# Optimization experiments

Measured on AMD Instinct MI355X. Metric: run time of the kernel, lower is better.

Reference implementation:

```python
import jax, jax.numpy as jnp
import numpy as np

C = 512
GROUPS = 8
EPS = 1e-5


def setup_inputs() -> dict:
    key = jax.random.key(0)
    ks = jax.random.split(key, 7)
    b, c, h, w = 32, C, 32, 32
    x = jax.random.normal(ks[0], (b, c, h, w), dtype=jnp.float32)
    norm_gamma = jnp.ones((c,), dtype=jnp.float32)
    norm_beta = jnp.zeros((c,), dtype=jnp.float32)
    # 1x1 convs == per-pixel linear layers; store as [out, in] matrices
    qkv_w = jax.random.normal(ks[1], (3 * c, c), dtype=jnp.float32) * (1.0 / np.sqrt(c))
    qkv_b = jnp.zeros((3 * c,), dtype=jnp.float32)
    out_w = jax.random.normal(ks[2], (c, c), dtype=jnp.float32) * (1.0 / np.sqrt(c))
    out_b = jnp.zeros((c,), dtype=jnp.float32)
    return {"x": x, "norm_gamma": norm_gamma, "norm_beta": norm_beta,
            "qkv_w": qkv_w, "qkv_b": qkv_b, "out_w": out_w, "out_b": out_b}


def group_norm(x, gamma, beta):
    b, c, h, w = x.shape
    xg = x.reshape(b, GROUPS, c // GROUPS, h, w)
    mean = jnp.mean(xg, axis=(2, 3, 4), keepdims=True)
    var = jnp.var(xg, axis=(2, 3, 4), keepdims=True)
    xg = (xg - mean) * jax.lax.rsqrt(var + EPS)
    x = xg.reshape(b, c, h, w)
    return x * gamma[None, :, None, None] + beta[None, :, None, None]


def reference(x, norm_gamma, norm_beta, qkv_w, qkv_b, out_w, out_b):
    b, c, h, w = x.shape
    xn = group_norm(x, norm_gamma, norm_beta)
    # 1x1 conv: [b,c,h,w] -> [b,3c,h,w]
    qkv = jnp.einsum('oc,bchw->bohw', qkv_w, xn) + qkv_b[None, :, None, None]
    q, k, v = jnp.split(qkv.reshape(b, 3 * c, h * w), 3, axis=1)  # each [b,c,hw]
    scale = c ** (-0.5)
    attn = jnp.einsum('bci,bcj->bij', q, k) * scale  # [b, hw, hw]
    attn = jax.nn.softmax(attn, axis=-1)
    out = jnp.einsum('bij,bcj->bci', attn, v).reshape(b, c, h, w)
    out = jnp.einsum('oc,bchw->bohw', out_w, out) + out_b[None, :, None, None]
    return x + out
```

## Files before the change

### kernel.cpp

```cpp
#include <hip/hip_runtime.h>

#define HW 1024
#define CD 512

typedef __bf16 bf16x8 __attribute__((ext_vector_type(8)));
typedef float f32x4 __attribute__((ext_vector_type(4)));

__device__ __forceinline__ unsigned short f2bf(float f) {
    unsigned int u = __float_as_uint(f);
    u += 0x7fff + ((u >> 16) & 1);
    return (unsigned short)(u >> 16);
}
__device__ __forceinline__ float bf2f(unsigned short h) {
    return __uint_as_float((unsigned)h << 16);
}

#define AS1(p) ((__attribute__((address_space(1))) void*)(p))
#define AS3(p) ((__attribute__((address_space(3))) void*)(p))
#define GLD16(gp, lp) __builtin_amdgcn_global_load_lds(AS1(gp), AS3(lp), 16, 0, 0)
#define WAITVM(n) do { asm volatile("s_waitcnt vmcnt(" #n ")" ::: "memory"); \
                       __builtin_amdgcn_sched_barrier(0); } while (0)

__global__ __launch_bounds__(256)
void gn_stats(const float* __restrict__ x, float* __restrict__ mean, float* __restrict__ rstd) {
    int bg = blockIdx.x;
    const float4* p4 = (const float4*)(x + (size_t)bg * 65536);
    int tid = threadIdx.x;
    float s = 0.f, ss = 0.f;
#pragma unroll 8
    for (int it = 0; it < 64; ++it) {
        float4 v = p4[tid + it * 256];
        s  += v.x + v.y + v.z + v.w;
        ss += v.x * v.x + v.y * v.y + v.z * v.z + v.w * v.w;
    }
#pragma unroll
    for (int d = 32; d > 0; d >>= 1) { s += __shfl_down(s, d); ss += __shfl_down(ss, d); }
    __shared__ float ls[4], lss[4];
    if ((tid & 63) == 0) { ls[tid >> 6] = s; lss[tid >> 6] = ss; }
    __syncthreads();
    if (tid == 0) {
        float S = ls[0] + ls[1] + ls[2] + ls[3];
        float SS = lss[0] + lss[1] + lss[2] + lss[3];
        float m = S * (1.f / 65536.f);
        float v = SS * (1.f / 65536.f) - m * m;
        mean[bg] = m;
        rstd[bg] = rsqrtf(v + 1e-5f);
    }
}

__global__ __launch_bounds__(256)
void gn_norm_t(const float* __restrict__ x, const float* __restrict__ mean, const float* __restrict__ rstd,
               const float* __restrict__ gamma, const float* __restrict__ beta,
               unsigned short* __restrict__ xnT) {
    __shared__ unsigned short tile[64][67];
    int i0 = blockIdx.x * 64, c0 = blockIdx.y * 64, b = blockIdx.z;
    float m = mean[b * 8 + blockIdx.y];
    float r = rstd[b * 8 + blockIdx.y];
    int tid = threadIdx.x;
    int tr = tid >> 4, tc = (tid & 15) * 4;
    const float* xb = x + ((size_t)b * CD + c0) * HW + i0;
#pragma unroll
    for (int p = 0; p < 4; ++p) {
        int c = tr + p * 16;
        float g = gamma[c0 + c] * r;
        float bb = beta[c0 + c] - m * g;
        float4 v = *(const float4*)(xb + (size_t)c * HW + tc);
        tile[c][tc + 0] = f2bf(v.x * g + bb);
        tile[c][tc + 1] = f2bf(v.y * g + bb);
        tile[c][tc + 2] = f2bf(v.z * g + bb);
        tile[c][tc + 3] = f2bf(v.w * g + bb);
    }
    __syncthreads();
    unsigned short* ob = xnT + ((size_t)b * HW + i0) * CD + c0;
#pragma unroll
    for (int p = 0; p < 4; ++p) {
        int ir = tr + p * 16;
        ushort4 u;
        u.x = tile[tc + 0][ir];
        u.y = tile[tc + 1][ir];
        u.z = tile[tc + 2][ir];
        u.w = tile[tc + 3][ir];
        *(ushort4*)(ob + (size_t)ir * CD + tc) = u;
    }
}

__global__ __launch_bounds__(256)
void tpose3_bf16(const float* __restrict__ qkv_w, unsigned short* __restrict__ dst0) {
    __shared__ unsigned short tile[64][67];
    const int zmap[3] = {0, 2, 1};
    const float* src = qkv_w + (size_t)blockIdx.z * CD * CD;
    unsigned short* dst = dst0 + (size_t)zmap[blockIdx.z] * CD * CD;
    int i0 = blockIdx.x * 64, c0 = blockIdx.y * 64;
    int tid = threadIdx.x;
    int tr = tid >> 4, tc = (tid & 15) * 4;
#pragma unroll
    for (int p = 0; p < 4; ++p) {
        int r = tr + p * 16;
        float4 v = *(const float4*)(src + (size_t)(i0 + r) * CD + c0 + tc);
        tile[r][tc + 0] = f2bf(v.x);
        tile[r][tc + 1] = f2bf(v.y);
        tile[r][tc + 2] = f2bf(v.z);
        tile[r][tc + 3] = f2bf(v.w);
    }
    __syncthreads();
#pragma unroll
    for (int p = 0; p < 4; ++p) {
        int ir = tr + p * 16;
        ushort4 u;
        u.x = tile[tc + 0][ir];
        u.y = tile[tc + 1][ir];
        u.z = tile[tc + 2][ir];
        u.w = tile[tc + 3][ir];
        *(ushort4*)(dst + (size_t)(c0 + ir) * CD + i0 + tc) = u;
    }
}

__global__ __launch_bounds__(256)
void cvt_bf16(const float* __restrict__ src, unsigned short* __restrict__ dst) {
    int i = blockIdx.x * 256 + threadIdx.x;
    float4 v = ((const float4*)src)[i];
    ushort4 u;
    u.x = f2bf(v.x); u.y = f2bf(v.y); u.z = f2bf(v.z); u.w = f2bf(v.w);
    ((ushort4*)dst)[i] = u;
}

__global__ __launch_bounds__(256)
void gvec_kernel(const float* __restrict__ wk, const float* __restrict__ bq,
                 float* __restrict__ g) {
    __shared__ float red[4][64];
    int d = blockIdx.x * 64 + (threadIdx.x & 63);
    int os = threadIdx.x >> 6;
    float acc = 0.f;
    for (int o = os * 128; o < os * 128 + 128; ++o)
        acc += wk[(size_t)o * CD + d] * bq[o];
    red[os][threadIdx.x & 63] = acc;
    __syncthreads();
    if (threadIdx.x < 64)
        g[blockIdx.x * 64 + threadIdx.x] = red[0][threadIdx.x] + red[1][threadIdx.x] +
                                           red[2][threadIdx.x] + red[3][threadIdx.x];
}

__global__ __launch_bounds__(256)
void bias2_kernel(const float* __restrict__ out_w, const float* __restrict__ bv,
                  float* __restrict__ bias2) {
    int wid = threadIdx.x >> 6, lane = threadIdx.x & 63;
    int o = blockIdx.x * 4 + wid;
    float acc = 0.f;
#pragma unroll
    for (int t = 0; t < 512; t += 64)
        acc += out_w[(size_t)o * CD + t + lane] * bv[t + lane];
#pragma unroll
    for (int d = 32; d > 0; d >>= 1) acc += __shfl_down(acc, d);
    if (lane == 0) bias2[o] = acc;
}

template<int EPI>
__global__ __launch_bounds__(512, 2)
void gemm8(const unsigned short* __restrict__ A, const unsigned short* __restrict__ B,
           unsigned short* __restrict__ C, const float* __restrict__ bias,
           int M, int N, int K, long long sA, long long sB, long long sC) {
    unsigned nx = gridDim.x, ny = gridDim.y;
    unsigned lin = blockIdx.x + nx * (blockIdx.y + ny * blockIdx.z);
    unsigned nwg = nx * ny * gridDim.z;
    unsigned work = (lin & 7) * (nwg >> 3) + (lin >> 3);
    unsigned bx = work % nx; work /= nx;
    unsigned by = work % ny;
    unsigned bz = work / ny;

    A += (size_t)bz * sA;
    B += (size_t)bz * sB;
    int m0 = by * 256, n0 = bx * 256;

    __shared__ unsigned short lA[2][256 * 64];
    __shared__ unsigned short lB[2][256 * 64];

    int tid = threadIdx.x, lane = tid & 63, wid = tid >> 6;
    int wr = wid >> 2, wc = wid & 3;

    f32x4 acc[8][4] = {};

    int strow[4], stcol[4];
#pragma unroll
    for (int s = 0; s < 4; ++s) {
        int idx = s * 512 + tid;
        strow[s] = idx >> 3;
        stcol[s] = ((idx & 7) ^ (strow[s] & 7)) * 8;
    }

    auto stage = [&](int buf, int kt) {
        int k0 = kt << 6;
#pragma unroll
        for (int s = 0; s < 4; ++s)
            GLD16(A + (size_t)(m0 + strow[s]) * K + k0 + stcol[s], &lA[buf][(size_t)(s * 512 + tid) * 8]);
#pragma unroll
        for (int s = 0; s < 4; ++s)
            GLD16(B + (size_t)(n0 + strow[s]) * K + k0 + stcol[s], &lB[buf][(size_t)(s * 512 + tid) * 8]);
    };

    int NT = K >> 6;
    stage(0, 0);
    if (NT > 1) stage(1, 1);

    for (int t = 0; t < NT; ++t) {
        if (t < NT - 1) WAITVM(8); else WAITVM(0);
        __builtin_amdgcn_s_barrier();
        const char* pa = (const char*)lA[t & 1];
        const char* pb = (const char*)lB[t & 1];
        __builtin_amdgcn_s_setprio(1);
#pragma unroll
        for (int kk = 0; kk < 64; kk += 32) {
            int koff = (kk + (lane >> 4) * 8) * 2;
            bf16x8 af[8], bfr[4];
#pragma unroll
            for (int m = 0; m < 8; ++m) {
                int row = wr * 128 + m * 16 + (lane & 15);
                af[m] = *(const bf16x8*)(pa + ((row * 128 + koff) ^ ((row & 7) << 4)));
            }
#pragma unroll
            for (int n = 0; n < 4; ++n) {
                int row = wc * 64 + n * 16 + (lane & 15);
                bfr[n] = *(const bf16x8*)(pb + ((row * 128 + koff) ^ ((row & 7) << 4)));
            }
#pragma unroll
            for (int m = 0; m < 8; ++m)
#pragma unroll
                for (int n = 0; n < 4; ++n)
                    acc[m][n] = __builtin_amdgcn_mfma_f32_16x16x32_bf16(af[m], bfr[n], acc[m][n], 0, 0, 0);
        }
        __builtin_amdgcn_s_setprio(0);
        __builtin_amdgcn_s_barrier();
        if (t + 2 < NT) stage(t & 1, t + 2);
    }

    int rl = (lane >> 4) * 4;
    int cl = lane & 15;
    unsigned short* Cb = C + (size_t)bz * sC;
#pragma unroll
    for (int m = 0; m < 8; ++m)
#pragma unroll
        for (int n = 0; n < 4; ++n) {
            int gm = m0 + wr * 128 + m * 16 + rl;
            int gn = n0 + wc * 64 + n * 16 + cl;
#pragma unroll
            for (int rg = 0; rg < 4; ++rg) {
                float v = acc[m][n][rg];
                if (EPI == 0) v += bias[gn];
                if (EPI == 1) v += bias[gm + rg];
                Cb[(size_t)(gm + rg) * N + gn] = f2bf(v);
            }
        }
}

template<int EPI>
__global__ __launch_bounds__(256, 2)
void gemm_bt(const unsigned short* __restrict__ A, const unsigned short* __restrict__ B,
             void* __restrict__ Cv, const float* __restrict__ bias,
             int M, int N, int K, long long sA, long long sB, long long sC) {
    unsigned nx = gridDim.x, ny = gridDim.y;
    unsigned lin = blockIdx.x + nx * (blockIdx.y + ny * blockIdx.z);
    unsigned nwg = nx * ny * gridDim.z;
    unsigned work = (lin & 7) * (nwg >> 3) + (lin >> 3);
    unsigned bx = work % nx; work /= nx;
    unsigned by = work % ny;
    unsigned bz = work / ny;

    A += (size_t)bz * sA;
    B += (size_t)bz * sB;
    int m0 = by * 128, n0 = bx * 128;

    __shared__ unsigned short lA[2][128 * 64];
    __shared__ unsigned short lB[2][128 * 64];

    int tid = threadIdx.x;
    int lane = tid & 63;
    int wr = (tid >> 6) >> 1, wc = (tid >> 6) & 1;

    f32x4 acc[4][4] = {};

    int strow[4], stcol[4];
#pragma unroll
    for (int s = 0; s < 4; ++s) {
        int row = (s * 256 + tid) >> 3;
        int g = (tid & 7) ^ (row & 7);
        strow[s] = row;
        stcol[s] = g * 8;
    }

    auto stage = [&](int buf, int k0) {
#pragma unroll
        for (int s = 0; s < 4; ++s) {
            GLD16(A + (size_t)(m0 + strow[s]) * K + k0 + stcol[s], &lA[buf][(size_t)(s * 256 + tid) * 8]);
            GLD16(B + (size_t)(n0 + strow[s]) * K + k0 + stcol[s], &lB[buf][(size_t)(s * 256 + tid) * 8]);
        }
    };

    int NT = K >> 6;
    stage(0, 0);
    __syncthreads();
    int cur = 0;
    for (int t = 0; t < NT; ++t) {
        if (t + 1 < NT) stage(cur ^ 1, (t + 1) << 6);
        const char* pa = (const char*)lA[cur];
        const char* pb = (const char*)lB[cur];
#pragma unroll
        for (int kk = 0; kk < 64; kk += 32) {
            bf16x8 af[4], bfr[4];
#pragma unroll
            for (int m = 0; m < 4; ++m) {
                int row = wr * 64 + m * 16 + (lane & 15);
                int off = (row * 128 + (kk + (lane >> 4) * 8) * 2) ^ ((row & 7) << 4);
                af[m] = *(const bf16x8*)(pa + off);
            }
#pragma unroll
            for (int n = 0; n < 4; ++n) {
                int row = wc * 64 + n * 16 + (lane & 15);
                int off = (row * 128 + (kk + (lane >> 4) * 8) * 2) ^ ((row & 7) << 4);
                bfr[n] = *(const bf16x8*)(pb + off);
            }
#pragma unroll
            for (int m = 0; m < 4; ++m)
#pragma unroll
                for (int n = 0; n < 4; ++n)
                    acc[m][n] = __builtin_amdgcn_mfma_f32_16x16x32_bf16(af[m], bfr[n], acc[m][n], 0, 0, 0);
        }
        __syncthreads();
        cur ^= 1;
    }

    int rl = (lane >> 4) * 4;
    int cl = lane & 15;
    unsigned short* Cb = (unsigned short*)Cv + (size_t)bz * sC;
#pragma unroll
    for (int m = 0; m < 4; ++m)
#pragma unroll
        for (int n = 0; n < 4; ++n) {
            int gm = m0 + wr * 64 + m * 16 + rl;
            int gn = n0 + wc * 64 + n * 16 + cl;
#pragma unroll
            for (int rg = 0; rg < 4; ++rg) {
                float v = acc[m][n][rg];
                if (EPI == 0) v += bias[gn];
                if (EPI == 1) v += bias[gm + rg];
                Cb[(size_t)(gm + rg) * N + gn] = f2bf(v);
            }
        }
}

__global__ __launch_bounds__(256, 2)
void scores_gemm(const unsigned short* __restrict__ T1, const unsigned short* __restrict__ xnT,
                 unsigned short* __restrict__ S, float* __restrict__ tmax, float* __restrict__ tsum) {
    unsigned nx = gridDim.x, ny = gridDim.y;
    unsigned lin = blockIdx.x + nx * (blockIdx.y + ny * blockIdx.z);
    unsigned nwg = nx * ny * gridDim.z;
    unsigned work = (lin & 7) * (nwg >> 3) + (lin >> 3);
    unsigned bx = work % nx; work /= nx;
    unsigned by = work % ny;
    unsigned bz = work / ny;

    const unsigned short* Ab = T1 + (size_t)bz * HW * CD;
    const unsigned short* Bb = xnT + (size_t)bz * HW * CD;
    int m0 = by * 128, n0 = bx * 128;

    __shared__ unsigned short lA[2][128 * 64];
    __shared__ unsigned short lB[2][128 * 64];
    __shared__ float redm[2][128];
    __shared__ float reds[2][128];

    int tid = threadIdx.x, lane = tid & 63;
    int wr = (tid >> 6) >> 1, wc = (tid >> 6) & 1;

    f32x4 acc[4][4] = {};
    int strow[4], stcol[4];
#pragma unroll
    for (int s = 0; s < 4; ++s) {
        int row = (s * 256 + tid) >> 3;
        int g = (tid & 7) ^ (row & 7);
        strow[s] = row;
        stcol[s] = g * 8;
    }

    auto stage = [&](int buf, int k0) {
#pragma unroll
        for (int s = 0; s < 4; ++s) {
            GLD16(Ab + (size_t)(m0 + strow[s]) * CD + k0 + stcol[s], &lA[buf][(size_t)(s * 256 + tid) * 8]);
            GLD16(Bb + (size_t)(n0 + strow[s]) * CD + k0 + stcol[s], &lB[buf][(size_t)(s * 256 + tid) * 8]);
        }
    };

    stage(0, 0);
    __syncthreads();
    int cur = 0;
    for (int t = 0; t < 8; ++t) {
        if (t < 7) stage(cur ^ 1, (t + 1) << 6);
        const char* pa = (const char*)lA[cur];
        const char* pb = (const char*)lB[cur];
#pragma unroll
        for (int kk = 0; kk < 64; kk += 32) {
            bf16x8 af[4], bfr[4];
#pragma unroll
            for (int m = 0; m < 4; ++m) {
                int row = wr * 64 + m * 16 + (lane & 15);
                int off = (row * 128 + (kk + (lane >> 4) * 8) * 2) ^ ((row & 7) << 4);
                af[m] = *(const bf16x8*)(pa + off);
            }
#pragma unroll
            for (int n = 0; n < 4; ++n) {
                int row = wc * 64 + n * 16 + (lane & 15);
                int off = (row * 128 + (kk + (lane >> 4) * 8) * 2) ^ ((row & 7) << 4);
                bfr[n] = *(const bf16x8*)(pb + off);
            }
#pragma unroll
            for (int m = 0; m < 4; ++m)
#pragma unroll
                for (int n = 0; n < 4; ++n)
                    acc[m][n] = __builtin_amdgcn_mfma_f32_16x16x32_bf16(af[m], bfr[n], acc[m][n], 0, 0, 0);
        }
        __syncthreads();
        cur ^= 1;
    }

    const float SL2E = 0.044194173824159216f * 1.4426950408889634f;
#pragma unroll
    for (int m = 0; m < 4; ++m)
#pragma unroll
        for (int n = 0; n < 4; ++n) acc[m][n] *= SL2E;

    int rl = (lane >> 4) * 4;
    int cl = lane & 15;

    float mr[4][4];
#pragma unroll
    for (int m = 0; m < 4; ++m)
#pragma unroll
        for (int rg = 0; rg < 4; ++rg)
            mr[m][rg] = fmaxf(fmaxf(acc[m][0][rg], acc[m][1][rg]),
                              fmaxf(acc[m][2][rg], acc[m][3][rg]));
#pragma unroll
    for (int d = 1; d < 16; d <<= 1)
#pragma unroll
        for (int m = 0; m < 4; ++m)
#pragma unroll
            for (int rg = 0; rg < 4; ++rg) mr[m][rg] = fmaxf(mr[m][rg], __shfl_xor(mr[m][rg], d));
    if ((lane & 15) == 0)
#pragma unroll
        for (int m = 0; m < 4; ++m)
#pragma unroll
            for (int rg = 0; rg < 4; ++rg) redm[wc][wr * 64 + m * 16 + rl + rg] = mr[m][rg];
    __syncthreads();
    float Mt[4][4];
#pragma unroll
    for (int m = 0; m < 4; ++m)
#pragma unroll
        for (int rg = 0; rg < 4; ++rg) {
            int row = wr * 64 + m * 16 + rl + rg;
            Mt[m][rg] = fmaxf(redm[0][row], redm[1][row]);
        }

    float sr[4][4] = {};
#pragma unroll
    for (int m = 0; m < 4; ++m)
#pragma unroll
        for (int n = 0; n < 4; ++n)
#pragma unroll
            for (int rg = 0; rg < 4; ++rg) {
                float e = __builtin_amdgcn_exp2f(acc[m][n][rg] - Mt[m][rg]);
                acc[m][n][rg] = e;
                sr[m][rg] += e;
            }
#pragma unroll
    for (int d = 1; d < 16; d <<= 1)
#pragma unroll
        for (int m = 0; m < 4; ++m)
#pragma unroll
            for (int rg = 0; rg < 4; ++rg) sr[m][rg] += __shfl_xor(sr[m][rg], d);
    if ((lane & 15) == 0)
#pragma unroll
        for (int m = 0; m < 4; ++m)
#pragma unroll
            for (int rg = 0; rg < 4; ++rg) reds[wc][wr * 64 + m * 16 + rl + rg] = sr[m][rg];
    __syncthreads();

    if (tid < 128) {
        float M = fmaxf(redm[0][tid], redm[1][tid]);
        float Z = reds[0][tid] + reds[1][tid];
        size_t o = ((size_t)bz * 8 + bx) * HW + m0 + tid;
        tmax[o] = M;
        tsum[o] = Z;
    }

    unsigned short* Sb = S + (size_t)bz * HW * HW;
#pragma unroll
    for (int m = 0; m < 4; ++m)
#pragma unroll
        for (int n = 0; n < 4; ++n) {
            int gm = m0 + wr * 64 + m * 16 + rl;
            int gn = n0 + wc * 64 + n * 16 + cl;
#pragma unroll
            for (int rg = 0; rg < 4; ++rg)
                Sb[(size_t)(gm + rg) * HW + gn] = f2bf(acc[m][n][rg]);
        }
}

__global__ __launch_bounds__(256)
void rescale_kernel(const float* __restrict__ tmax, const float* __restrict__ tsum,
                    float* __restrict__ ratio) {
    int r = blockIdx.x * 256 + threadIdx.x;
    int b = r >> 10, i = r & 1023;
    const float* tm = tmax + (size_t)b * 8 * HW + i;
    const float* ts = tsum + (size_t)b * 8 * HW + i;
    float M = -1e30f;
#pragma unroll
    for (int jt = 0; jt < 8; ++jt) M = fmaxf(M, tm[(size_t)jt * HW]);
    float Z = 0.f;
#pragma unroll
    for (int jt = 0; jt < 8; ++jt) Z += ts[(size_t)jt * HW] * __builtin_amdgcn_exp2f(tm[(size_t)jt * HW] - M);
    float rZ = 1.0f / Z;
#pragma unroll
    for (int jt = 0; jt < 7; ++jt)
        ratio[((size_t)b * 8 + jt) * HW + i] =
            __builtin_amdgcn_exp2f(tm[(size_t)jt * HW] - tm[(size_t)(jt + 1) * HW]);
    ratio[((size_t)b * 8 + 7) * HW + i] = __builtin_amdgcn_exp2f(tm[(size_t)7 * HW] - M) * rZ;
}

__global__ __launch_bounds__(256)
void pv_gemm(const unsigned short* __restrict__ A, const unsigned short* __restrict__ B,
             float* __restrict__ C, const float* __restrict__ bias,
             const float* __restrict__ resid, const float* __restrict__ ratio) {
    unsigned nx = gridDim.x, ny = gridDim.y;
    unsigned lin = blockIdx.x + nx * (blockIdx.y + ny * blockIdx.z);
    unsigned nwg = nx * ny * gridDim.z;
    unsigned work = (lin & 7) * (nwg >> 3) + (lin >> 3);
    unsigned bx = work % nx; work /= nx;
    unsigned by = work % ny;
    unsigned bz = work / ny;

    A += (size_t)bz * 512 * 1024;
    B += (size_t)bz * 1024 * 1024;
    int m0 = by * 128, n0 = bx * 128;

    __shared__ unsigned short lA[2][128 * 64];
    __shared__ unsigned short lB[2][128 * 64];

    int tid = threadIdx.x, lane = tid & 63;
    int wr = (tid >> 6) >> 1, wc = (tid >> 6) & 1;
    int cl = lane & 15;

    f32x4 acc[4][4] = {};

    int strow[4], stcol[4];
#pragma unroll
    for (int s = 0; s < 4; ++s) {
        int row = (s * 256 + tid) >> 3;
        int g = (tid & 7) ^ (row & 7);
        strow[s] = row;
        stcol[s] = g * 8;
    }

    auto stage = [&](int buf, int k0) {
#pragma unroll
        for (int s = 0; s < 4; ++s) {
            GLD16(A + (size_t)(m0 + strow[s]) * 1024 + k0 + stcol[s], &lA[buf][(size_t)(s * 256 + tid) * 8]);
            GLD16(B + (size_t)(n0 + strow[s]) * 1024 + k0 + stcol[s], &lB[buf][(size_t)(s * 256 + tid) * 8]);
        }
    };

    const float* rbase = ratio + (size_t)bz * 8 * HW + n0 + wc * 64 + cl;

    stage(0, 0);
    __syncthreads();
    int cur = 0;
    float r0 = 0.f, r1 = 0.f, r2 = 0.f, r3 = 0.f;
    for (int t = 0; t < 16; ++t) {
        if (t + 1 < 16) stage(cur ^ 1, (t + 1) << 6);
        if (!(t & 1)) {
            int jt = t >> 1;
            r0 = rbase[(size_t)jt * HW + 0];
            r1 = rbase[(size_t)jt * HW + 16];
            r2 = rbase[(size_t)jt * HW + 32];
            r3 = rbase[(size_t)jt * HW + 48];
        }
        const char* pa = (const char*)lA[cur];
        const char* pb = (const char*)lB[cur];
#pragma unroll
        for (int kk = 0; kk < 64; kk += 32) {
            bf16x8 af[4], bfr[4];
#pragma unroll
            for (int m = 0; m < 4; ++m) {
                int row = wr * 64 + m * 16 + (lane & 15);
                int off = (row * 128 + (kk + (lane >> 4) * 8) * 2) ^ ((row & 7) << 4);
                af[m] = *(const bf16x8*)(pa + off);
            }
#pragma unroll
            for (int n = 0; n < 4; ++n) {
                int row = wc * 64 + n * 16 + (lane & 15);
                int off = (row * 128 + (kk + (lane >> 4) * 8) * 2) ^ ((row & 7) << 4);
                bfr[n] = *(const bf16x8*)(pb + off);
            }
#pragma unroll
            for (int m = 0; m < 4; ++m)
#pragma unroll
                for (int n = 0; n < 4; ++n)
                    acc[m][n] = __builtin_amdgcn_mfma_f32_16x16x32_bf16(af[m], bfr[n], acc[m][n], 0, 0, 0);
        }
        __syncthreads();
        cur ^= 1;
        if (t & 1) {
#pragma unroll
            for (int m = 0; m < 4; ++m) {
                acc[m][0] *= r0;
                acc[m][1] *= r1;
                acc[m][2] *= r2;
                acc[m][3] *= r3;
            }
        }
    }

    int rl = (lane >> 4) * 4;
    float* Cf = C + (size_t)bz * 512 * 1024;
    const float* Rs = resid + (size_t)bz * 512 * 1024;
#pragma unroll
    for (int m = 0; m < 4; ++m)
#pragma unroll
        for (int n = 0; n < 4; ++n) {
            int gm = m0 + wr * 64 + m * 16 + rl;
            int gn = n0 + wc * 64 + n * 16 + cl;
#pragma unroll
            for (int rg = 0; rg < 4; ++rg) {
                size_t off = (size_t)(gm + rg) * 1024 + gn;
                Cf[off] = acc[m][n][rg] + bias[gm + rg] + Rs[off];
            }
        }
}

extern "C" void kernel_launch(void* const* d_in, const int* in_sizes, int n_in,
                              void* d_out, int out_size, void* d_ws, size_t ws_size,
                              hipStream_t stream) {
    const float* x      = (const float*)d_in[0];
    const float* gamma  = (const float*)d_in[1];
    const float* beta   = (const float*)d_in[2];
    const float* qkv_w  = (const float*)d_in[3];
    const float* qkv_b  = (const float*)d_in[4];
    const float* out_w  = (const float*)d_in[5];
    const float* out_b  = (const float*)d_in[6];

    char* ws = (char*)d_ws;
    unsigned short* xnT  = (unsigned short*)ws;
    unsigned short* vpr  = (unsigned short*)(ws + 33554432);
    unsigned short* SP   = (unsigned short*)(ws + 67108864);
    unsigned short* wqkT = (unsigned short*)(ws + 100663296);
    unsigned short* w2   = (unsigned short*)(ws + 101187584);
    float* gvec          = (float*)(ws + 101711872);
    float* bias2         = (float*)(ws + 101713920);
    float* meanp         = (float*)(ws + 101715968);
    float* rstdp         = (float*)(ws + 101716992);
    float* tmaxp         = (float*)(ws + 101718016);
    float* tsump         = (float*)(ws + 102766592);
    float* ratiop        = (float*)(ws + 103815168);

    unsigned short* slot0 = SP;
    unsigned short* owb   = SP + 786432;

    unsigned short* T1 = (unsigned short*)((char*)d_out + 33554432);
    float* outF = (float*)d_out;

    const float* wk_f = qkv_w + (size_t)512 * CD;

    gn_stats<<<256, 256, 0, stream>>>(x, meanp, rstdp);
    gn_norm_t<<<dim3(16, 8, 32), 256, 0, stream>>>(x, meanp, rstdp, gamma, beta, xnT);

    tpose3_bf16<<<dim3(8, 8, 3), 256, 0, stream>>>(qkv_w, slot0);
    cvt_bf16<<<256, 256, 0, stream>>>(out_w, owb);
    gvec_kernel<<<8, 256, 0, stream>>>(wk_f, qkv_b, gvec);
    bias2_kernel<<<128, 256, 0, stream>>>(out_w, qkv_b + 1024, bias2);

    gemm_bt<3><<<dim3(4, 4, 2), 256, 0, stream>>>(slot0 + 524288, slot0, wqkT, nullptr,
        512, 512, 512, 262144, 262144, 262144);

    gemm8<0><<<dim3(2, 4, 32), 512, 0, stream>>>(xnT, wqkT, T1, gvec,
        1024, 512, 512, 1024LL * 512, 0, 1024LL * 512);
    gemm8<1><<<dim3(4, 2, 32), 512, 0, stream>>>(w2, xnT, vpr, bias2,
        512, 1024, 512, 0, 1024LL * 512, 512LL * 1024);

    for (int h = 0; h < 2; ++h) {
        const unsigned short* T1h = T1 + (size_t)h * 16 * 1024 * 512;
        const unsigned short* xh  = xnT + (size_t)h * 16 * 1024 * 512;
        float* tmaxh = tmaxp + (size_t)h * 16 * 8 * 1024;
        float* tsumh = tsump + (size_t)h * 16 * 8 * 1024;

        scores_gemm<<<dim3(8, 8, 16), 256, 0, stream>>>(T1h, xh, SP, tmaxh, tsumh);
        rescale_kernel<<<64, 256, 0, stream>>>(tmaxh, tsumh, ratiop);
        pv_gemm<<<dim3(8, 4, 16), 256, 0, stream>>>(
            vpr + (size_t)h * 16 * 512 * 1024, SP,
            outF + (size_t)h * 16 * 512 * 1024, out_b,
            x + (size_t)h * 16 * 512 * 1024, ratiop);
    }
    (void)in_sizes; (void)n_in; (void)out_size; (void)ws_size;
}
```

Measured before the change: 220.6 us.

## Replace scores GEMM with 256x256-tile 8-wave kernel and coarser softmax partials

Replaces the 128x128-tile scores kernel with a 512-thread, 256x256-tile version that uses a two-stage prefetch pipeline with explicit vmcnt waits and raised wave priority around the MFMA loop. Because each block now covers 256 key columns, the per-row max/sum partials drop from 8 to 4 column tiles, so rescale_kernel and pv_gemm's ratio indexing are adjusted to apply rescaling every 4 K-steps instead of every 2. The larger tile is meant to raise arithmetic intensity and cut global/LDS traffic per FLOP. In exchange it uses 64KB of LDS for operand buffers plus more accumulator registers, which may reduce occupancy, and the grid shrinks to 256 blocks per half.

New measurement: 218.5 us (median of 2 runs). No clear change (-1.0%).

```diff
diff --git a/kernel.cpp b/kernel.cpp
--- a/kernel.cpp
+++ b/kernel.cpp
@@ -251,6 +251,167 @@
         }
 }
 
+__global__ __launch_bounds__(512, 2)
+void scores8(const unsigned short* __restrict__ T1, const unsigned short* __restrict__ xnT,
+             unsigned short* __restrict__ S, float* __restrict__ tmax, float* __restrict__ tsum) {
+    unsigned nx = gridDim.x, ny = gridDim.y;
+    unsigned lin = blockIdx.x + nx * (blockIdx.y + ny * blockIdx.z);
+    unsigned nwg = nx * ny * gridDim.z;
+    unsigned work = (lin & 7) * (nwg >> 3) + (lin >> 3);
+    unsigned bx = work % nx; work /= nx;
+    unsigned by = work % ny;
+    unsigned bz = work / ny;
+
+    const unsigned short* Ab = T1 + (size_t)bz * HW * CD;
+    const unsigned short* Bb = xnT + (size_t)bz * HW * CD;
+    int m0 = by * 256, n0 = bx * 256;
+
+    __shared__ unsigned short lA[2][256 * 64];
+    __shared__ unsigned short lB[2][256 * 64];
+    __shared__ float redm[4][256];
+    __shared__ float reds[4][256];
+
+    int tid = threadIdx.x, lane = tid & 63, wid = tid >> 6;
+    int wr = wid >> 2, wc = wid & 3;
+
+    f32x4 acc[8][4] = {};
+
+    int strow[4], stcol[4];
+#pragma unroll
+    for (int s = 0; s < 4; ++s) {
+        int idx = s * 512 + tid;
+        strow[s] = idx >> 3;
+        stcol[s] = ((idx & 7) ^ (strow[s] & 7)) * 8;
+    }
+
+    auto stage = [&](int buf, int kt) {
+        int k0 = kt << 6;
+#pragma unroll
+        for (int s = 0; s < 4; ++s)
+            GLD16(Ab + (size_t)(m0 + strow[s]) * CD + k0 + stcol[s], &lA[buf][(size_t)(s * 512 + tid) * 8]);
+#pragma unroll
+        for (int s = 0; s < 4; ++s)
+            GLD16(Bb + (size_t)(n0 + strow[s]) * CD + k0 + stcol[s], &lB[buf][(size_t)(s * 512 + tid) * 8]);
+    };
+
+    stage(0, 0);
+    stage(1, 1);
+
+    for (int t = 0; t < 8; ++t) {
+        if (t < 7) WAITVM(8); else WAITVM(0);
+        __builtin_amdgcn_s_barrier();
+        const char* pa = (const char*)lA[t & 1];
+        const char* pb = (const char*)lB[t & 1];
+        __builtin_amdgcn_s_setprio(1);
+#pragma unroll
+        for (int kk = 0; kk < 64; kk += 32) {
+            int koff = (kk + (lane >> 4) * 8) * 2;
+            bf16x8 af[8], bfr[4];
+#pragma unroll
+            for (int m = 0; m < 8; ++m) {
+                int row = wr * 128 + m * 16 + (lane & 15);
+                af[m] = *(const bf16x8*)(pa + ((row * 128 + koff) ^ ((row & 7) << 4)));
+            }
+#pragma unroll
+            for (int n = 0; n < 4; ++n) {
+                int row = wc * 64 + n * 16 + (lane & 15);
+                bfr[n] = *(const bf16x8*)(pb + ((row * 128 + koff) ^ ((row & 7) << 4)));
+            }
+#pragma unroll
+            for (int m = 0; m < 8; ++m)
+#pragma unroll
+                for (int n = 0; n < 4; ++n)
+                    acc[m][n] = __builtin_amdgcn_mfma_f32_16x16x32_bf16(af[m], bfr[n], acc[m][n], 0, 0, 0);
+        }
+        __builtin_amdgcn_s_setprio(0);
+        __builtin_amdgcn_s_barrier();
+        if (t + 2 < 8) stage(t & 1, t + 2);
+    }
+
+    const float SL2E = 0.044194173824159216f * 1.4426950408889634f;
+#pragma unroll
+    for (int m = 0; m < 8; ++m)
+#pragma unroll
+        for (int n = 0; n < 4; ++n) acc[m][n] *= SL2E;
+
+    int rl = (lane >> 4) * 4;
+    int cl = lane & 15;
+
+    float mr[8][4];
+#pragma unroll
+    for (int m = 0; m < 8; ++m)
+#pragma unroll
+        for (int rg = 0; rg < 4; ++rg)
+            mr[m][rg] = fmaxf(fmaxf(acc[m][0][rg], acc[m][1][rg]),
+                              fmaxf(acc[m][2][rg], acc[m][3][rg]));
+#pragma unroll
+    for (int d = 1; d < 16; d <<= 1)
+#pragma unroll
+        for (int m = 0; m < 8; ++m)
+#pragma unroll
+            for (int rg = 0; rg < 4; ++rg) mr[m][rg] = fmaxf(mr[m][rg], __shfl_xor(mr[m][rg], d));
+    if ((lane & 15) == 0)
+#pragma unroll
+        for (int m = 0; m < 8; ++m)
+#pragma unroll
+            for (int rg = 0; rg < 4; ++rg) redm[wc][wr * 128 + m * 16 + rl + rg] = mr[m][rg];
+    __syncthreads();
+    float Mt[8][4];
+#pragma unroll
+    for (int m = 0; m < 8; ++m)
+#pragma unroll
+        for (int rg = 0; rg < 4; ++rg) {
+            int row = wr * 128 + m * 16 + rl + rg;
+            Mt[m][rg] = fmaxf(fmaxf(redm[0][row], redm[1][row]),
+                              fmaxf(redm[2][row], redm[3][row]));
+        }
+
+    float sr[8][4] = {};
+#pragma unroll
+    for (int m = 0; m < 8; ++m)
+#pragma unroll
+        for (int n = 0; n < 4; ++n)
+#pragma unroll
+            for (int rg = 0; rg < 4; ++rg) {
+                float e = __builtin_amdgcn_exp2f(acc[m][n][rg] - Mt[m][rg]);
+                acc[m][n][rg] = e;
+                sr[m][rg] += e;
+            }
+#pragma unroll
+    for (int d = 1; d < 16; d <<= 1)
+#pragma unroll
+        for (int m = 0; m < 8; ++m)
+#pragma unroll
+            for (int rg = 0; rg < 4; ++rg) sr[m][rg] += __shfl_xor(sr[m][rg], d);
+    if ((lane & 15) == 0)
+#pragma unroll
+        for (int m = 0; m < 8; ++m)
+#pragma unroll
+            for (int rg = 0; rg < 4; ++rg) reds[wc][wr * 128 + m * 16 + rl + rg] = sr[m][rg];
+    __syncthreads();
+
+    if (tid < 256) {
+        float M = fmaxf(fmaxf(redm[0][tid], redm[1][tid]),
+                        fmaxf(redm[2][tid], redm[3][tid]));
+        float Z = reds[0][tid] + reds[1][tid] + reds[2][tid] + reds[3][tid];
+        size_t o = ((size_t)bz * 4 + bx) * HW + m0 + tid;
+        tmax[o] = M;
+        tsum[o] = Z;
+    }
+
+    unsigned short* Sb = S + (size_t)bz * HW * HW;
+#pragma unroll
+    for (int m = 0; m < 8; ++m)
+#pragma unroll
+        for (int n = 0; n < 4; ++n) {
+            int gm = m0 + wr * 128 + m * 16 + rl;
+            int gn = n0 + wc * 64 + n * 16 + cl;
+#pragma unroll
+            for (int rg = 0; rg < 4; ++rg)
+                Sb[(size_t)(gm + rg) * HW + gn] = f2bf(acc[m][n][rg]);
+        }
+}
+
 template<int EPI>
 __global__ __launch_bounds__(256, 2)
 void gemm_bt(const unsigned short* __restrict__ A, const unsigned short* __restrict__ B,
@@ -346,180 +507,25 @@
         }
 }
 
-__global__ __launch_bounds__(256, 2)
-void scores_gemm(const unsigned short* __restrict__ T1, const unsigned short* __restrict__ xnT,
-                 unsigned short* __restrict__ S, float* __restrict__ tmax, float* __restrict__ tsum) {
-    unsigned nx = gridDim.x, ny = gridDim.y;
-    unsigned lin = blockIdx.x + nx * (blockIdx.y + ny * blockIdx.z);
-    unsigned nwg = nx * ny * gridDim.z;
-    unsigned work = (lin & 7) * (nwg >> 3) + (lin >> 3);
-    unsigned bx = work % nx; work /= nx;
-    unsigned by = work % ny;
-    unsigned bz = work / ny;
-
-    const unsigned short* Ab = T1 + (size_t)bz * HW * CD;
-    const unsigned short* Bb = xnT + (size_t)bz * HW * CD;
-    int m0 = by * 128, n0 = bx * 128;
-
-    __shared__ unsigned short lA[2][128 * 64];
-    __shared__ unsigned short lB[2][128 * 64];
-    __shared__ float redm[2][128];
-    __shared__ float reds[2][128];
-
-    int tid = threadIdx.x, lane = tid & 63;
-    int wr = (tid >> 6) >> 1, wc = (tid >> 6) & 1;
-
-    f32x4 acc[4][4] = {};
-    int strow[4], stcol[4];
-#pragma unroll
-    for (int s = 0; s < 4; ++s) {
-        int row = (s * 256 + tid) >> 3;
-        int g = (tid & 7) ^ (row & 7);
-        strow[s] = row;
-        stcol[s] = g * 8;
-    }
-
-    auto stage = [&](int buf, int k0) {
-#pragma unroll
-        for (int s = 0; s < 4; ++s) {
-            GLD16(Ab + (size_t)(m0 + strow[s]) * CD + k0 + stcol[s], &lA[buf][(size_t)(s * 256 + tid) * 8]);
-            GLD16(Bb + (size_t)(n0 + strow[s]) * CD + k0 + stcol[s], &lB[buf][(size_t)(s * 256 + tid) * 8]);
-        }
-    };
-
-    stage(0, 0);
-    __syncthreads();
-    int cur = 0;
-    for (int t = 0; t < 8; ++t) {
-        if (t < 7) stage(cur ^ 1, (t + 1) << 6);
-        const char* pa = (const char*)lA[cur];
-        const char* pb = (const char*)lB[cur];
-#pragma unroll
-        for (int kk = 0; kk < 64; kk += 32) {
-            bf16x8 af[4], bfr[4];
-#pragma unroll
-            for (int m = 0; m < 4; ++m) {
-                int row = wr * 64 + m * 16 + (lane & 15);
-                int off = (row * 128 + (kk + (lane >> 4) * 8) * 2) ^ ((row & 7) << 4);
-                af[m] = *(const bf16x8*)(pa + off);
-            }
-#pragma unroll
-            for (int n = 0; n < 4; ++n) {
-                int row = wc * 64 + n * 16 + (lane & 15);
-                int off = (row * 128 + (kk + (lane >> 4) * 8) * 2) ^ ((row & 7) << 4);
-                bfr[n] = *(const bf16x8*)(pb + off);
-            }
-#pragma unroll
-            for (int m = 0; m < 4; ++m)
-#pragma unroll
-                for (int n = 0; n < 4; ++n)
-                    acc[m][n] = __builtin_amdgcn_mfma_f32_16x16x32_bf16(af[m], bfr[n], acc[m][n], 0, 0, 0);
-        }
-        __syncthreads();
-        cur ^= 1;
-    }
-
-    const float SL2E = 0.044194173824159216f * 1.4426950408889634f;
-#pragma unroll
-    for (int m = 0; m < 4; ++m)
-#pragma unroll
-        for (int n = 0; n < 4; ++n) acc[m][n] *= SL2E;
-
-    int rl = (lane >> 4) * 4;
-    int cl = lane & 15;
-
-    float mr[4][4];
-#pragma unroll
-    for (int m = 0; m < 4; ++m)
-#pragma unroll
-        for (int rg = 0; rg < 4; ++rg)
-            mr[m][rg] = fmaxf(fmaxf(acc[m][0][rg], acc[m][1][rg]),
-                              fmaxf(acc[m][2][rg], acc[m][3][rg]));
-#pragma unroll
-    for (int d = 1; d < 16; d <<= 1)
-#pragma unroll
-        for (int m = 0; m < 4; ++m)
-#pragma unroll
-            for (int rg = 0; rg < 4; ++rg) mr[m][rg] = fmaxf(mr[m][rg], __shfl_xor(mr[m][rg], d));
-    if ((lane & 15) == 0)
-#pragma unroll
-        for (int m = 0; m < 4; ++m)
-#pragma unroll
-            for (int rg = 0; rg < 4; ++rg) redm[wc][wr * 64 + m * 16 + rl + rg] = mr[m][rg];
-    __syncthreads();
-    float Mt[4][4];
-#pragma unroll
-    for (int m = 0; m < 4; ++m)
-#pragma unroll
-        for (int rg = 0; rg < 4; ++rg) {
-            int row = wr * 64 + m * 16 + rl + rg;
-            Mt[m][rg] = fmaxf(redm[0][row], redm[1][row]);
-        }
-
-    float sr[4][4] = {};
-#pragma unroll
-    for (int m = 0; m < 4; ++m)
-#pragma unroll
-        for (int n = 0; n < 4; ++n)
-#pragma unroll
-            for (int rg = 0; rg < 4; ++rg) {
-                float e = __builtin_amdgcn_exp2f(acc[m][n][rg] - Mt[m][rg]);
-                acc[m][n][rg] = e;
-                sr[m][rg] += e;
-            }
-#pragma unroll
-    for (int d = 1; d < 16; d <<= 1)
-#pragma unroll
-        for (int m = 0; m < 4; ++m)
-#pragma unroll
-            for (int rg = 0; rg < 4; ++rg) sr[m][rg] += __shfl_xor(sr[m][rg], d);
-    if ((lane & 15) == 0)
-#pragma unroll
-        for (int m = 0; m < 4; ++m)
-#pragma unroll
-            for (int rg = 0; rg < 4; ++rg) reds[wc][wr * 64 + m * 16 + rl + rg] = sr[m][rg];
-    __syncthreads();
-
-    if (tid < 128) {
-        float M = fmaxf(redm[0][tid], redm[1][tid]);
-        float Z = reds[0][tid] + reds[1][tid];
-        size_t o = ((size_t)bz * 8 + bx) * HW + m0 + tid;
-        tmax[o] = M;
-        tsum[o] = Z;
-    }
-
-    unsigned short* Sb = S + (size_t)bz * HW * HW;
-#pragma unroll
-    for (int m = 0; m < 4; ++m)
-#pragma unroll
-        for (int n = 0; n < 4; ++n) {
-            int gm = m0 + wr * 64 + m * 16 + rl;
-            int gn = n0 + wc * 64 + n * 16 + cl;
-#pragma unroll
-            for (int rg = 0; rg < 4; ++rg)
-                Sb[(size_t)(gm + rg) * HW + gn] = f2bf(acc[m][n][rg]);
-        }
-}
-
 __global__ __launch_bounds__(256)
 void rescale_kernel(const float* __restrict__ tmax, const float* __restrict__ tsum,
                     float* __restrict__ ratio) {
     int r = blockIdx.x * 256 + threadIdx.x;
     int b = r >> 10, i = r & 1023;
-    const float* tm = tmax + (size_t)b * 8 * HW + i;
-    const float* ts = tsum + (size_t)b * 8 * HW + i;
+    const float* tm = tmax + (size_t)b * 4 * HW + i;
+    const float* ts = tsum + (size_t)b * 4 * HW + i;
     float M = -1e30f;
 #pragma unroll
-    for (int jt = 0; jt < 8; ++jt) M = fmaxf(M, tm[(size_t)jt * HW]);
+    for (int jt = 0; jt < 4; ++jt) M = fmaxf(M, tm[(size_t)jt * HW]);
     float Z = 0.f;
 #pragma unroll
-    for (int jt = 0; jt < 8; ++jt) Z += ts[(size_t)jt * HW] * __builtin_amdgcn_exp2f(tm[(size_t)jt * HW] - M);
+    for (int jt = 0; jt < 4; ++jt) Z += ts[(size_t)jt * HW] * __builtin_amdgcn_exp2f(tm[(size_t)jt * HW] - M);
     float rZ = 1.0f / Z;
 #pragma unroll
-    for (int jt = 0; jt < 7; ++jt)
-        ratio[((size_t)b * 8 + jt) * HW + i] =
+    for (int jt = 0; jt < 3; ++jt)
+        ratio[((size_t)b * 4 + jt) * HW + i] =
             __builtin_amdgcn_exp2f(tm[(size_t)jt * HW] - tm[(size_t)(jt + 1) * HW]);
-    ratio[((size_t)b * 8 + 7) * HW + i] = __builtin_amdgcn_exp2f(tm[(size_t)7 * HW] - M) * rZ;
+    ratio[((size_t)b * 4 + 3) * HW + i] = __builtin_amdgcn_exp2f(tm[(size_t)3 * HW] - M) * rZ;
 }
 
 __global__ __launch_bounds__(256)
@@ -564,7 +570,7 @@
         }
     };
 
-    const float* rbase = ratio + (size_t)bz * 8 * HW + n0 + wc * 64 + cl;
+    const float* rbase = ratio + (size_t)bz * 4 * HW + n0 + wc * 64 + cl;
 
     stage(0, 0);
     __syncthreads();
@@ -572,8 +578,8 @@
     float r0 = 0.f, r1 = 0.f, r2 = 0.f, r3 = 0.f;
     for (int t = 0; t < 16; ++t) {
         if (t + 1 < 16) stage(cur ^ 1, (t + 1) << 6);
-        if (!(t & 1)) {
-            int jt = t >> 1;
+        if (!(t & 3)) {
+            int jt = t >> 2;
             r0 = rbase[(size_t)jt * HW + 0];
             r1 = rbase[(size_t)jt * HW + 16];
             r2 = rbase[(size_t)jt * HW + 32];
@@ -604,7 +610,7 @@
         }
         __syncthreads();
         cur ^= 1;
-        if (t & 1) {
+        if ((t & 3) == 3) {
 #pragma unroll
             for (int m = 0; m < 4; ++m) {
                 acc[m][0] *= r0;
@@ -684,10 +690,10 @@
     for (int h = 0; h < 2; ++h) {
         const unsigned short* T1h = T1 + (size_t)h * 16 * 1024 * 512;
         const unsigned short* xh  = xnT + (size_t)h * 16 * 1024 * 512;
-        float* tmaxh = tmaxp + (size_t)h * 16 * 8 * 1024;
-        float* tsumh = tsump + (size_t)h * 16 * 8 * 1024;
-
-        scores_gemm<<<dim3(8, 8, 16), 256, 0, stream>>>(T1h, xh, SP, tmaxh, tsumh);
+        float* tmaxh = tmaxp + (size_t)h * 16 * 4 * 1024;
+        float* tsumh = tsump + (size_t)h * 16 * 4 * 1024;
+
+        scores8<<<dim3(4, 4, 16), 512, 0, stream>>>(T1h, xh, SP, tmaxh, tsumh);
         rescale_kernel<<<64, 256, 0, stream>>>(tmaxh, tsumh, ratiop);
         pv_gemm<<<dim3(8, 4, 16), 256, 0, stream>>>(
             vpr + (size_t)h * 16 * 512 * 1024, SP,
```
